# Optimization experiments

Hardware: AMD Instinct MI355X
Metric: run time of the kernel (lower is better)

## Reference

```python
import jax, jax.numpy as jnp
import numpy as np

N_NODES = 100000


def sage_conv(x, src, dst, W_l, b_l, W_r):
    # PyG SAGEConv (aggr='mean'): out = lin_l(mean_j x_j) + lin_r(x_i)
    msg = x[src]  # [E, d] gather of source-node features
    agg = jax.ops.segment_sum(msg, dst, num_segments=N_NODES)  # [N, d]
    deg = jax.ops.segment_sum(jnp.ones((src.shape[0],), x.dtype), dst,
                              num_segments=N_NODES)
    mean = agg / jnp.clip(deg, 1.0, None)[:, None]
    return mean @ W_l.T + b_l + x @ W_r.T


def setup_inputs() -> dict:
    key = jax.random.key(0)
    ks = jax.random.split(key, 12)
    d_in, d_h, d_out, n_edges = 64, 64, 2, 1200000
    s = 1.0 / np.sqrt(d_h)
    inp = {
        "x": jax.random.normal(ks[0], (N_NODES, d_in), dtype=jnp.float32),
        "edge_index": jax.random.randint(ks[1], (2, n_edges), 0, N_NODES,
                                         dtype=jnp.int64),
        "W_l1": jax.random.uniform(ks[2], (d_h, d_in), jnp.float32, -s, s),
        "b_l1": jax.random.uniform(ks[3], (d_h,), jnp.float32, -s, s),
        "W_r1": jax.random.uniform(ks[4], (d_h, d_in), jnp.float32, -s, s),
        "W_l2": jax.random.uniform(ks[5], (d_h, d_h), jnp.float32, -s, s),
        "b_l2": jax.random.uniform(ks[6], (d_h,), jnp.float32, -s, s),
        "W_r2": jax.random.uniform(ks[7], (d_h, d_h), jnp.float32, -s, s),
        "W_c": jax.random.uniform(ks[8], (d_out, d_h), jnp.float32, -s, s),
        "b_c": jax.random.uniform(ks[9], (d_out,), jnp.float32, -s, s),
    }
    return inp


def reference(x, edge_index, W_l1, b_l1, W_r1, W_l2, b_l2, W_r2, W_c, b_c):
    src, dst = edge_index[0], edge_index[1]
    # layer 1 + relu (dropout is identity in eval mode)
    h = jax.nn.relu(sage_conv(x, src, dst, W_l1, b_l1, W_r1))
    # layer 2 (no relu per forward())
    h = sage_conv(h, src, dst, W_l2, b_l2, W_r2)
    # classifier
    return h @ W_c.T + b_c
```

## Files before the change

kernel.cpp:

```cpp
#include <hip/hip_runtime.h>

#define N_NODES 100000
#define D 64
#define NTILES 3125
#define NBUCK 391
#define NBLK_A 256
#define GCNT_N (NBUCK * NBLK_A)
#define NCHUNK ((GCNT_N + 255) / 256)
#define NTILE_T (N_NODES / 32)
#define TROW 72
#define TBLK 512

typedef __attribute__((ext_vector_type(8))) short short8;
typedef __attribute__((ext_vector_type(16))) float f32x16;
union Pack8 { uint4 u; short8 s; };

__device__ __forceinline__ unsigned f2bf(float f) {
  unsigned u = __float_as_uint(f);
  return (u + 0x7fffu + ((u >> 16) & 1u)) >> 16;
}
#define BF_LO(u) __uint_as_float(((unsigned)(u)) << 16)
#define BF_HI(u) __uint_as_float(((unsigned)(u)) & 0xffff0000u)



__global__ __launch_bounds__(256) void passA_count(const int* __restrict__ dst,
                                                   int* __restrict__ gcnt,
                                                   int nE, int ec) {
  __shared__ int cnt[NBUCK];
  int t = threadIdx.x, blk = blockIdx.x;
  for (int i = t; i < NBUCK; i += 256) cnt[i] = 0;
  __syncthreads();
  int e0 = blk * ec, e1 = min(e0 + ec, nE);
  for (int e = e0 + t; e < e1; e += 256) atomicAdd(&cnt[dst[e] >> 8], 1);
  __syncthreads();
  for (int b = t; b < NBUCK; b += 256) gcnt[b * NBLK_A + blk] = cnt[b];
}

__global__ void gscan_p1(const int* __restrict__ g, int* __restrict__ csum) {
  int t = threadIdx.x, b = blockIdx.x;
  int i = b * 256 + t;
  int v = (i < GCNT_N) ? g[i] : 0;
  for (int off = 32; off; off >>= 1) v += __shfl_down(v, off);
  __shared__ int ws4[4];
  if ((t & 63) == 0) ws4[t >> 6] = v;
  __syncthreads();
  if (t == 0) csum[b] = ws4[0] + ws4[1] + ws4[2] + ws4[3];
}

__global__ void gscan_p2(int* __restrict__ csum, int nB) {
  __shared__ int s[1024];
  int t = threadIdx.x;
  int orig = (t < nB) ? csum[t] : 0;
  s[t] = orig;
  __syncthreads();
  for (int off = 1; off < 1024; off <<= 1) {
    int v = (t >= off) ? s[t - off] : 0;
    __syncthreads();
    s[t] += v;
    __syncthreads();
  }
  if (t < nB) csum[t] = s[t] - orig;
}

__global__ void gscan_p3(int* __restrict__ g, const int* __restrict__ csum) {
  __shared__ int s[256];
  int t = threadIdx.x, b = blockIdx.x;
  int i = b * 256 + t;
  int d = (i < GCNT_N) ? g[i] : 0;
  s[t] = d;
  __syncthreads();
  for (int off = 1; off < 256; off <<= 1) {
    int v = (t >= off) ? s[t - off] : 0;
    __syncthreads();
    s[t] += v;
    __syncthreads();
  }
  if (i < GCNT_N) g[i] = s[t] - d + csum[b];
}

__global__ __launch_bounds__(256) void passC_prep(
    const int* __restrict__ src, const int* __restrict__ dst,
    const int* __restrict__ S, unsigned* __restrict__ pairs4, int nE, int ec,
    const float* __restrict__ Wc, const float* __restrict__ Wl2,
    const float* __restrict__ Wr2, const float* __restrict__ bl2,
    const float* __restrict__ bc, const float* __restrict__ Wl1,
    const float* __restrict__ Wr1, float* __restrict__ A2,
    float* __restrict__ B2, float* __restrict__ bfv,
    unsigned short* __restrict__ wcat) {
  __shared__ int cur[NBUCK];
  int t = threadIdx.x, blk = blockIdx.x;
  if (blk < NBLK_A) {
    for (int b = t; b < NBUCK; b += 256) cur[b] = S[b * NBLK_A + blk];
    __syncthreads();
    int e0 = blk * ec, e1 = min(e0 + ec, nE);
    for (int e = e0 + t; e < e1; e += 256) {
      int d = dst[e];
      int p = atomicAdd(&cur[d >> 8], 1);
      pairs4[p] = ((unsigned)(d & 255) << 24) | (unsigned)src[e];
    }
  } else {
    for (int i = t; i < 8192; i += 256)
      wcat[i] = (unsigned short)f2bf((i < 4096) ? Wl1[i] : Wr1[i - 4096]);
    if (t < 128) {
      int c = t >> 6, k = t & 63;
      float sa = 0.f, sb = 0.f;
      for (int j = 0; j < 64; ++j) {
        float w = Wc[c * 64 + j];
        sa = fmaf(w, Wl2[j * 64 + k], sa);
        sb = fmaf(w, Wr2[j * 64 + k], sb);
      }
      A2[c * 64 + k] = sa;
      B2[c * 64 + k] = sb;
    }
    if (t < 2) {
      float s = bc[t];
      for (int j = 0; j < 64; ++j) s = fmaf(Wc[t * 64 + j], bl2[j], s);
      bfv[t] = s;
    }
  }
}

__global__ __launch_bounds__(256) void passD_transform(
    const unsigned* __restrict__ pairs4, const int* __restrict__ S,
    int* __restrict__ tstart, unsigned* __restrict__ srt4, int nE,
    const float* __restrict__ x, const unsigned short* __restrict__ wcat,
    const float* __restrict__ bl, unsigned short* __restrict__ t1,
    unsigned short* __restrict__ r1b) {
  __shared__ int h8[8 * 16];
  __shared__ int ex8[9];
  __shared__ int cur8[8];
  int t = threadIdx.x;
  if (blockIdx.x < NBUCK) {
    int b = blockIdx.x;
    int base = S[b * NBLK_A];
    int end = (b == NBUCK - 1) ? nE : S[(b + 1) * NBLK_A];
    if (t < 128) h8[t] = 0;
    __syncthreads();
    for (int p = base + t; p < end; p += 256)
      atomicAdd(&h8[((pairs4[p] >> 29) & 7) * 16 + (t & 15)], 1);
    __syncthreads();
    if (t == 0) {
      int run = base;
      for (int bin = 0; bin < 8; ++bin) {
        ex8[bin] = run;
        int s = 0;
        for (int i = 0; i < 16; ++i) s += h8[bin * 16 + i];
        run += s;
      }
      ex8[8] = run;
    }
    __syncthreads();
    if (t < 8) {
      cur8[t] = ex8[t];
      tstart[b * 8 + t] = ex8[t];
    }
    if (b == NBUCK - 1 && t == 0) tstart[NBUCK * 8] = nE;
    __syncthreads();
    for (int p = base + t; p < end; p += 256) {
      unsigned pk = pairs4[p];
      int slot = atomicAdd(&cur8[(pk >> 29) & 7], 1);
      srt4[slot] = pk;
    }
  } else {
    int lane = t & 63;
    int l31 = lane & 31, hi = lane >> 5;

    short8 af[4][4];
#pragma unroll
    for (int jt = 0; jt < 4; ++jt)
#pragma unroll
      for (int kk = 0; kk < 4; ++kk)
        af[jt][kk] =
            *(const short8*)(wcat + (jt * 32 + l31) * 64 + kk * 16 + 8 * hi);

    const f32x16 Z = {0.f, 0.f, 0.f, 0.f, 0.f, 0.f, 0.f, 0.f,
                      0.f, 0.f, 0.f, 0.f, 0.f, 0.f, 0.f, 0.f};
    const float4* x4 = (const float4*)x;

    int gw = ((blockIdx.x - NBUCK) * 256 + t) >> 6;
    int nW = (TBLK * 256) >> 6;

    for (int tile = gw; tile < NTILE_T; tile += nW) {
      int node = tile * 32 + l31;
      f32x16 acc[4] = {Z, Z, Z, Z};
#pragma unroll
      for (int kk = 0; kk < 4; ++kk) {
        float4 fa = x4[(size_t)node * 16 + kk * 4 + 2 * hi];
        float4 fb = x4[(size_t)node * 16 + kk * 4 + 2 * hi + 1];
        Pack8 pk;
        pk.u.x = f2bf(fa.x) | (f2bf(fa.y) << 16);
        pk.u.y = f2bf(fa.z) | (f2bf(fa.w) << 16);
        pk.u.z = f2bf(fb.x) | (f2bf(fb.y) << 16);
        pk.u.w = f2bf(fb.z) | (f2bf(fb.w) << 16);
        acc[0] = __builtin_amdgcn_mfma_f32_32x32x16_bf16(af[0][kk], pk.s, acc[0], 0, 0, 0);
        acc[1] = __builtin_amdgcn_mfma_f32_32x32x16_bf16(af[1][kk], pk.s, acc[1], 0, 0, 0);
        acc[2] = __builtin_amdgcn_mfma_f32_32x32x16_bf16(af[2][kk], pk.s, acc[2], 0, 0, 0);
        acc[3] = __builtin_amdgcn_mfma_f32_32x32x16_bf16(af[3][kk], pk.s, acc[3], 0, 0, 0);
      }
#pragma unroll
      for (int jt = 0; jt < 2; ++jt)
#pragma unroll
        for (int rg = 0; rg < 4; ++rg) {
          int j0 = jt * 32 + 8 * rg + 4 * hi;
          uint2 p;
          p.x = f2bf(acc[jt][4 * rg + 0]) | (f2bf(acc[jt][4 * rg + 1]) << 16);
          p.y = f2bf(acc[jt][4 * rg + 2]) | (f2bf(acc[jt][4 * rg + 3]) << 16);
          *(uint2*)(t1 + (size_t)node * 64 + j0) = p;
        }
#pragma unroll
      for (int jt = 2; jt < 4; ++jt)
#pragma unroll
        for (int rg = 0; rg < 4; ++rg) {
          int j0 = (jt - 2) * 32 + 8 * rg + 4 * hi;
          float4 bv = ((const float4*)bl)[j0 >> 2];
          uint2 p;
          p.x = f2bf(acc[jt][4 * rg + 0] + bv.x) |
                (f2bf(acc[jt][4 * rg + 1] + bv.y) << 16);
          p.y = f2bf(acc[jt][4 * rg + 2] + bv.z) |
                (f2bf(acc[jt][4 * rg + 3] + bv.w) << 16);
          *(uint2*)(r1b + (size_t)node * 64 + j0) = p;
        }
    }
  }
}

__global__ __launch_bounds__(256) void tile_g1(
    const unsigned* __restrict__ srt4, const int* __restrict__ tstart,
    const unsigned short* __restrict__ t1,
    const unsigned short* __restrict__ r1b, const float* __restrict__ A2,
    const float* __restrict__ B2, float2* __restrict__ g2,
    float2* __restrict__ s2, int nE) {
  __shared__ float pAB[4][64];
  __shared__ unsigned short stg[4][2][16 * TROW];
  __shared__ int ideg[4][64];
  int t = threadIdx.x, lane = t & 63, w = t >> 6;
  pAB[t >> 6][t & 63] = (t < 128) ? A2[t] : B2[t - 128];
  __syncthreads();

  int tile = blockIdx.x;
  int base = tstart[tile];
  int end = tstart[tile + 1];
  int l31 = lane & 31, hi = lane >> 5;
  int o = lane >> 3, j8 = lane & 7;
  unsigned short* stA = &stg[w][0][0];
  unsigned short* stB = &stg[w][1][0];

  int ngAll = (end > base) ? ((end - base + 15) >> 4) : 0;
  int gper = (ngAll + 3) >> 2;
  int wbase = base + min(w * gper, ngAll) * 16;
  int wend = min(base + min((w + 1) * gper, ngAll) * 16, end);

  const f32x16 Z = {0.f, 0.f, 0.f, 0.f, 0.f, 0.f, 0.f, 0.f,
                    0.f, 0.f, 0.f, 0.f, 0.f, 0.f, 0.f, 0.f};
  f32x16 acc0 = Z, acc1 = Z;
  int degc = 0;
  int ng = (wend > wbase) ? ((wend - wbase + 15) >> 4) : 0;

  unsigned pkA = 0u, pkB = 0u;
  int cntA = 0, cntB = 0;
  uint4 vA0 = make_uint4(0, 0, 0, 0), vA1 = vA0, vB0 = vA0, vB1 = vA0;
  if (ng > 0) {
    pkA = srt4[min(wbase + (lane & 15), nE - 1)];
    cntA = min(wend - wbase, 16);
    int s0 = __shfl((int)pkA, o) & 0xFFFFFF;
    int s1 = __shfl((int)pkA, 8 + o) & 0xFFFFFF;
    vA0 = *(const uint4*)(t1 + (size_t)((o < cntA) ? s0 : 0) * 64 + j8 * 8);
    vA1 = *(const uint4*)(t1 + (size_t)((8 + o < cntA) ? s1 : 0) * 64 + j8 * 8);
  }
  if (ng > 1) {
    int nb = wbase + 16;
    pkB = srt4[min(nb + (lane & 15), nE - 1)];
    cntB = min(wend - nb, 16);
    int s0 = __shfl((int)pkB, o) & 0xFFFFFF;
    int s1 = __shfl((int)pkB, 8 + o) & 0xFFFFFF;
    vB0 = *(const uint4*)(t1 + (size_t)((o < cntB) ? s0 : 0) * 64 + j8 * 8);
    vB1 = *(const uint4*)(t1 + (size_t)((8 + o < cntB) ? s1 : 0) * 64 + j8 * 8);
  }

  for (int gg = 0; gg < ng; gg += 2) {
    bool hasB = (gg + 1 < ng);
    *(uint4*)(stA + o * TROW + j8 * 8) = vA0;
    *(uint4*)(stA + (8 + o) * TROW + j8 * 8) = vA1;
    if (hasB) {
      *(uint4*)(stB + o * TROW + j8 * 8) = vB0;
      *(uint4*)(stB + (8 + o) * TROW + j8 * 8) = vB1;
    }
    unsigned amA[8], amB[8];
#pragma unroll
    for (int m = 0; m < 8; ++m) {
      int e = 8 * hi + m;
      int pv = __shfl((int)pkA, e);
      bool ok = (e < cntA) && (((pv >> 24) & 31) == l31);
      amA[m] = ok ? 0x3F80u : 0u;
      degc += (amA[m] >> 7) & 1;
    }
    if (hasB) {
#pragma unroll
      for (int m = 0; m < 8; ++m) {
        int e = 8 * hi + m;
        int pv = __shfl((int)pkB, e);
        bool ok = (e < cntB) && (((pv >> 24) & 31) == l31);
        amB[m] = ok ? 0x3F80u : 0u;
        degc += (amB[m] >> 7) & 1;
      }
    }
    if (gg + 2 < ng) {
      int nb = wbase + (gg + 2) * 16;
      pkA = srt4[min(nb + (lane & 15), nE - 1)];
      cntA = min(wend - nb, 16);
      int s0 = __shfl((int)pkA, o) & 0xFFFFFF;
      int s1 = __shfl((int)pkA, 8 + o) & 0xFFFFFF;
      vA0 = *(const uint4*)(t1 + (size_t)((o < cntA) ? s0 : 0) * 64 + j8 * 8);
      vA1 = *(const uint4*)(t1 + (size_t)((8 + o < cntA) ? s1 : 0) * 64 + j8 * 8);
    }
    if (gg + 3 < ng) {
      int nb = wbase + (gg + 3) * 16;
      pkB = srt4[min(nb + (lane & 15), nE - 1)];
      cntB = min(wend - nb, 16);
      int s0 = __shfl((int)pkB, o) & 0xFFFFFF;
      int s1 = __shfl((int)pkB, 8 + o) & 0xFFFFFF;
      vB0 = *(const uint4*)(t1 + (size_t)((o < cntB) ? s0 : 0) * 64 + j8 * 8);
      vB1 = *(const uint4*)(t1 + (size_t)((8 + o < cntB) ? s1 : 0) * 64 + j8 * 8);
    }
    {
      Pack8 I;
      I.u.x = amA[0] | (amA[1] << 16);
      I.u.y = amA[2] | (amA[3] << 16);
      I.u.z = amA[4] | (amA[5] << 16);
      I.u.w = amA[6] | (amA[7] << 16);
      unsigned short b0[8], b1[8];
#pragma unroll
      for (int m = 0; m < 8; ++m) {
        b0[m] = stA[(8 * hi + m) * TROW + l31];
        b1[m] = stA[(8 * hi + m) * TROW + 32 + l31];
      }
      Pack8 F0, F1;
      F0.u.x = b0[0] | ((unsigned)b0[1] << 16);
      F0.u.y = b0[2] | ((unsigned)b0[3] << 16);
      F0.u.z = b0[4] | ((unsigned)b0[5] << 16);
      F0.u.w = b0[6] | ((unsigned)b0[7] << 16);
      F1.u.x = b1[0] | ((unsigned)b1[1] << 16);
      F1.u.y = b1[2] | ((unsigned)b1[3] << 16);
      F1.u.z = b1[4] | ((unsigned)b1[5] << 16);
      F1.u.w = b1[6] | ((unsigned)b1[7] << 16);
      acc0 = __builtin_amdgcn_mfma_f32_32x32x16_bf16(F0.s, I.s, acc0, 0, 0, 0);
      acc1 = __builtin_amdgcn_mfma_f32_32x32x16_bf16(F1.s, I.s, acc1, 0, 0, 0);
    }
    if (hasB) {
      Pack8 I;
      I.u.x = amB[0] | (amB[1] << 16);
      I.u.y = amB[2] | (amB[3] << 16);
      I.u.z = amB[4] | (amB[5] << 16);
      I.u.w = amB[6] | (amB[7] << 16);
      unsigned short b0[8], b1[8];
#pragma unroll
      for (int m = 0; m < 8; ++m) {
        b0[m] = stB[(8 * hi + m) * TROW + l31];
        b1[m] = stB[(8 * hi + m) * TROW + 32 + l31];
      }
      Pack8 F0, F1;
      F0.u.x = b0[0] | ((unsigned)b0[1] << 16);
      F0.u.y = b0[2] | ((unsigned)b0[3] << 16);
      F0.u.z = b0[4] | ((unsigned)b0[5] << 16);
      F0.u.w = b0[6] | ((unsigned)b0[7] << 16);
      F1.u.x = b1[0] | ((unsigned)b1[1] << 16);
      F1.u.y = b1[2] | ((unsigned)b1[3] << 16);
      F1.u.z = b1[4] | ((unsigned)b1[5] << 16);
      F1.u.w = b1[6] | ((unsigned)b1[7] << 16);
      acc0 = __builtin_amdgcn_mfma_f32_32x32x16_bf16(F0.s, I.s, acc0, 0, 0, 0);
      acc1 = __builtin_amdgcn_mfma_f32_32x32x16_bf16(F1.s, I.s, acc1, 0, 0, 0);
    }
  }

  ideg[w][lane] = degc;
  __syncthreads();
  float* red = (float*)&stg[0][0][0];
  for (int r = 1; r < 4; ++r) {
    if (w == r) {
#pragma unroll
      for (int i = 0; i < 16; ++i) {
        red[i * 64 + lane] = acc0[i];
        red[(16 + i) * 64 + lane] = acc1[i];
      }
    }
    __syncthreads();
    if (w == 0) {
#pragma unroll
      for (int i = 0; i < 16; ++i) {
        acc0[i] += red[i * 64 + lane];
        acc1[i] += red[(16 + i) * 64 + lane];
      }
    }
    __syncthreads();
  }

  if (w == 0) {
    int dtot = ideg[0][lane] + ideg[1][lane] + ideg[2][lane] + ideg[3][lane];
    float degf = (float)(dtot + __shfl_xor(dtot, 32));
    float inv = 1.f / fmaxf(degf, 1.f);
    int node = tile * 32 + l31;
    float d0 = 0.f, d1 = 0.f, d2 = 0.f, d3 = 0.f;
#pragma unroll
    for (int fb = 0; fb < 2; ++fb) {
#pragma unroll
      for (int q4 = 0; q4 < 4; ++q4) {
        int f0 = fb * 32 + q4 * 8 + 4 * hi;
        uint2 rv = *(const uint2*)(r1b + (size_t)node * 64 + f0);
        float bias[4] = {BF_LO(rv.x), BF_HI(rv.x), BF_LO(rv.y), BF_HI(rv.y)};
#pragma unroll
        for (int j = 0; j < 4; ++j) {
          float a = fb ? acc1[q4 * 4 + j] : acc0[q4 * 4 + j];
          float hv = fmaxf(fmaf(a, inv, bias[j]), 0.f);
          int f = f0 + j;
          d0 = fmaf(hv, pAB[0][f], d0);
          d1 = fmaf(hv, pAB[1][f], d1);
          d2 = fmaf(hv, pAB[2][f], d2);
          d3 = fmaf(hv, pAB[3][f], d3);
        }
      }
    }
    d0 += __shfl_xor(d0, 32);
    d1 += __shfl_xor(d1, 32);
    d2 += __shfl_xor(d2, 32);
    d3 += __shfl_xor(d3, 32);
    if (hi == 0) {
      g2[node] = make_float2(d0, d1);
      s2[node] = make_float2(d2, d3);
    }
  }
}

__global__ __launch_bounds__(256) void bucket_g2(
    const unsigned* __restrict__ pairs4, const int* __restrict__ S,
    const float2* __restrict__ g2, const float2* __restrict__ s2,
    const float* __restrict__ bfv, float* __restrict__ out, int nE) {
  __shared__ float o0[256], o1[256];
  __shared__ int cnt[256];
  int t = threadIdx.x, b = blockIdx.x;
  o0[t] = 0.f;
  o1[t] = 0.f;
  cnt[t] = 0;
  __syncthreads();
  int base = S[b * NBLK_A];
  int end = (b == NBUCK - 1) ? nE : S[(b + 1) * NBLK_A];
  for (int p = base + t; p < end; p += 256) {
    unsigned pk = pairs4[p];
    float2 v = g2[pk & 0xFFFFFFu];
    int dl = pk >> 24;
    atomicAdd(&o0[dl], v.x);
    atomicAdd(&o1[dl], v.y);
    atomicAdd(&cnt[dl], 1);
  }
  __syncthreads();
  int node = b * 256 + t;
  if (node < N_NODES) {
    float inv = 1.f / (float)max(cnt[t], 1);
    float2 sv = s2[node];
    out[(size_t)node * 2 + 0] = fmaf(o0[t], inv, sv.x) + bfv[0];
    out[(size_t)node * 2 + 1] = fmaf(o1[t], inv, sv.y) + bfv[1];
  }
}

extern "C" void kernel_launch(void* const* d_in, const int* in_sizes, int n_in,
                              void* d_out, int out_size, void* d_ws,
                              size_t ws_size, hipStream_t stream) {
  const float* x   = (const float*)d_in[0];
  const int*   ei  = (const int*)d_in[1];
  const float* Wl1 = (const float*)d_in[2];
  const float* bl1 = (const float*)d_in[3];
  const float* Wr1 = (const float*)d_in[4];
  const float* Wl2 = (const float*)d_in[5];
  const float* bl2 = (const float*)d_in[6];
  const float* Wr2 = (const float*)d_in[7];
  const float* Wc  = (const float*)d_in[8];
  const float* bc  = (const float*)d_in[9];
  float* out = (float*)d_out;

  int nE = in_sizes[1] / 2;
  const int* src = ei;
  const int* dst = ei + nE;

  unsigned* pairs4 = (unsigned*)d_ws;
  unsigned* srt4 = pairs4 + nE;
  unsigned short* t1 = (unsigned short*)(srt4 + nE);
  unsigned short* r1b = t1 + (size_t)N_NODES * D;
  float2* g2 = (float2*)(r1b + (size_t)N_NODES * D);
  float2* s2 = g2 + N_NODES;
  float* A2 = (float*)(s2 + N_NODES);
  float* B2 = A2 + 128;
  float* bfv = B2 + 128;
  unsigned short* wcat = (unsigned short*)(bfv + 4);
  int* tstart = (int*)(wcat + 8192);
  int* gcnt = tstart + (NBUCK * 8 + 2);
  int* csum = gcnt + GCNT_N;

  int ec = (nE + NBLK_A - 1) / NBLK_A;

  passA_count<<<NBLK_A, 256, 0, stream>>>(dst, gcnt, nE, ec);
  gscan_p1<<<NCHUNK, 256, 0, stream>>>(gcnt, csum);
  gscan_p2<<<1, 1024, 0, stream>>>(csum, NCHUNK);
  gscan_p3<<<NCHUNK, 256, 0, stream>>>(gcnt, csum);
  passC_prep<<<NBLK_A + 1, 256, 0, stream>>>(src, dst, gcnt, pairs4, nE, ec,
                                             Wc, Wl2, Wr2, bl2, bc, Wl1, Wr1,
                                             A2, B2, bfv, wcat);
  passD_transform<<<NBUCK + TBLK, 256, 0, stream>>>(pairs4, gcnt, tstart,
                                                    srt4, nE, x, wcat, bl1,
                                                    t1, r1b);
  tile_g1<<<NTILES, 256, 0, stream>>>(srt4, tstart, t1, r1b, A2, B2, g2, s2,
                                      nE);
  bucket_g2<<<NBUCK, 256, 0, stream>>>(pairs4, gcnt, g2, s2, bfv, out, nE);
}
```

Baseline: 124.5 us.

## Replace three-kernel global scan with atomic bucket offsets and in-block scan

Each counting block now reserves its slot within each bucket by atomically adding its count to a per-bucket total, which yields a per-block offset directly. The three separate scan kernels are removed, and the scatter kernel instead does a small 391-entry prefix scan in shared memory in every block to get bucket base addresses. This cuts two kernel launches and the global scan traffic, at the cost of a memset, global atomics, and a redundant per-block scan. Edge order within a bucket now depends on atomic arrival order, so results may differ slightly between runs through float summation order.

```diff
diff --git a/kernel.cpp b/kernel.cpp
--- a/kernel.cpp
+++ b/kernel.cpp
@@ -6,7 +6,6 @@
 #define NBUCK 391
 #define NBLK_A 256
 #define GCNT_N (NBUCK * NBLK_A)
-#define NCHUNK ((GCNT_N + 255) / 256)
 #define NTILE_T (N_NODES / 32)
 #define TROW 72
 #define TBLK 512
@@ -23,9 +22,9 @@
 #define BF_HI(u) __uint_as_float(((unsigned)(u)) & 0xffff0000u)
 
 
-
 __global__ __launch_bounds__(256) void passA_count(const int* __restrict__ dst,
-                                                   int* __restrict__ gcnt,
+                                                   int* __restrict__ goff,
+                                                   int* __restrict__ btot,
                                                    int nE, int ec) {
   __shared__ int cnt[NBUCK];
   int t = threadIdx.x, blk = blockIdx.x;
@@ -34,54 +33,14 @@
   int e0 = blk * ec, e1 = min(e0 + ec, nE);
   for (int e = e0 + t; e < e1; e += 256) atomicAdd(&cnt[dst[e] >> 8], 1);
   __syncthreads();
-  for (int b = t; b < NBUCK; b += 256) gcnt[b * NBLK_A + blk] = cnt[b];
-}
-
-__global__ void gscan_p1(const int* __restrict__ g, int* __restrict__ csum) {
-  int t = threadIdx.x, b = blockIdx.x;
-  int i = b * 256 + t;
-  int v = (i < GCNT_N) ? g[i] : 0;
-  for (int off = 32; off; off >>= 1) v += __shfl_down(v, off);
-  __shared__ int ws4[4];
-  if ((t & 63) == 0) ws4[t >> 6] = v;
-  __syncthreads();
-  if (t == 0) csum[b] = ws4[0] + ws4[1] + ws4[2] + ws4[3];
-}
-
-__global__ void gscan_p2(int* __restrict__ csum, int nB) {
-  __shared__ int s[1024];
-  int t = threadIdx.x;
-  int orig = (t < nB) ? csum[t] : 0;
-  s[t] = orig;
-  __syncthreads();
-  for (int off = 1; off < 1024; off <<= 1) {
-    int v = (t >= off) ? s[t - off] : 0;
-    __syncthreads();
-    s[t] += v;
-    __syncthreads();
-  }
-  if (t < nB) csum[t] = s[t] - orig;
-}
-
-__global__ void gscan_p3(int* __restrict__ g, const int* __restrict__ csum) {
-  __shared__ int s[256];
-  int t = threadIdx.x, b = blockIdx.x;
-  int i = b * 256 + t;
-  int d = (i < GCNT_N) ? g[i] : 0;
-  s[t] = d;
-  __syncthreads();
-  for (int off = 1; off < 256; off <<= 1) {
-    int v = (t >= off) ? s[t - off] : 0;
-    __syncthreads();
-    s[t] += v;
-    __syncthreads();
-  }
-  if (i < GCNT_N) g[i] = s[t] - d + csum[b];
+  for (int b = t; b < NBUCK; b += 256)
+    goff[b * NBLK_A + blk] = atomicAdd(&btot[b], cnt[b]);
 }
 
 __global__ __launch_bounds__(256) void passC_prep(
     const int* __restrict__ src, const int* __restrict__ dst,
-    const int* __restrict__ S, unsigned* __restrict__ pairs4, int nE, int ec,
+    const int* __restrict__ goff, const int* __restrict__ btot,
+    int* __restrict__ bstart, unsigned* __restrict__ pairs4, int nE, int ec,
     const float* __restrict__ Wc, const float* __restrict__ Wl2,
     const float* __restrict__ Wr2, const float* __restrict__ bl2,
     const float* __restrict__ bc, const float* __restrict__ Wl1,
@@ -89,9 +48,25 @@
     float* __restrict__ B2, float* __restrict__ bfv,
     unsigned short* __restrict__ wcat) {
   __shared__ int cur[NBUCK];
+  __shared__ int sa[512], sb[512];
   int t = threadIdx.x, blk = blockIdx.x;
   if (blk < NBLK_A) {
-    for (int b = t; b < NBUCK; b += 256) cur[b] = S[b * NBLK_A + blk];
+    for (int i = t; i < 512; i += 256) sa[i] = (i < NBUCK) ? btot[i] : 0;
+    __syncthreads();
+    int* A = sa;
+    int* B = sb;
+    for (int off = 1; off < 512; off <<= 1) {
+      for (int i = t; i < 512; i += 256)
+        B[i] = A[i] + ((i >= off) ? A[i - off] : 0);
+      __syncthreads();
+      int* tmp = A; A = B; B = tmp;
+    }
+    for (int b = t; b < NBUCK; b += 256) {
+      int base = (b == 0) ? 0 : A[b - 1];
+      cur[b] = base + goff[b * NBLK_A + blk];
+      if (blk == 0) bstart[b] = base;
+    }
+    if (blk == 0 && t == 0) bstart[NBUCK] = A[NBUCK - 1];
     __syncthreads();
     int e0 = blk * ec, e1 = min(e0 + ec, nE);
     for (int e = e0 + t; e < e1; e += 256) {
@@ -104,14 +79,14 @@
       wcat[i] = (unsigned short)f2bf((i < 4096) ? Wl1[i] : Wr1[i - 4096]);
     if (t < 128) {
       int c = t >> 6, k = t & 63;
-      float sa = 0.f, sb = 0.f;
+      float sa2 = 0.f, sb2 = 0.f;
       for (int j = 0; j < 64; ++j) {
         float w = Wc[c * 64 + j];
-        sa = fmaf(w, Wl2[j * 64 + k], sa);
-        sb = fmaf(w, Wr2[j * 64 + k], sb);
-      }
-      A2[c * 64 + k] = sa;
-      B2[c * 64 + k] = sb;
+        sa2 = fmaf(w, Wl2[j * 64 + k], sa2);
+        sb2 = fmaf(w, Wr2[j * 64 + k], sb2);
+      }
+      A2[c * 64 + k] = sa2;
+      B2[c * 64 + k] = sb2;
     }
     if (t < 2) {
       float s = bc[t];
@@ -122,7 +97,7 @@
 }
 
 __global__ __launch_bounds__(256) void passD_transform(
-    const unsigned* __restrict__ pairs4, const int* __restrict__ S,
+    const unsigned* __restrict__ pairs4, const int* __restrict__ bstart,
     int* __restrict__ tstart, unsigned* __restrict__ srt4, int nE,
     const float* __restrict__ x, const unsigned short* __restrict__ wcat,
     const float* __restrict__ bl, unsigned short* __restrict__ t1,
@@ -133,8 +108,8 @@
   int t = threadIdx.x;
   if (blockIdx.x < NBUCK) {
     int b = blockIdx.x;
-    int base = S[b * NBLK_A];
-    int end = (b == NBUCK - 1) ? nE : S[(b + 1) * NBLK_A];
+    int base = bstart[b];
+    int end = bstart[b + 1];
     if (t < 128) h8[t] = 0;
     __syncthreads();
     for (int p = base + t; p < end; p += 256)
@@ -432,7 +407,7 @@
 }
 
 __global__ __launch_bounds__(256) void bucket_g2(
-    const unsigned* __restrict__ pairs4, const int* __restrict__ S,
+    const unsigned* __restrict__ pairs4, const int* __restrict__ bstart,
     const float2* __restrict__ g2, const float2* __restrict__ s2,
     const float* __restrict__ bfv, float* __restrict__ out, int nE) {
   __shared__ float o0[256], o1[256];
@@ -442,8 +417,8 @@
   o1[t] = 0.f;
   cnt[t] = 0;
   __syncthreads();
-  int base = S[b * NBLK_A];
-  int end = (b == NBUCK - 1) ? nE : S[(b + 1) * NBLK_A];
+  int base = bstart[b];
+  int end = bstart[b + 1];
   for (int p = base + t; p < end; p += 256) {
     unsigned pk = pairs4[p];
     float2 v = g2[pk & 0xFFFFFFu];
@@ -492,22 +467,22 @@
   float* bfv = B2 + 128;
   unsigned short* wcat = (unsigned short*)(bfv + 4);
   int* tstart = (int*)(wcat + 8192);
-  int* gcnt = tstart + (NBUCK * 8 + 2);
-  int* csum = gcnt + GCNT_N;
+  int* goff = tstart + (NBUCK * 8 + 2);
+  int* btot = goff + GCNT_N;
+  int* bstart = btot + (NBUCK + 1);
 
   int ec = (nE + NBLK_A - 1) / NBLK_A;
 
-  passA_count<<<NBLK_A, 256, 0, stream>>>(dst, gcnt, nE, ec);
-  gscan_p1<<<NCHUNK, 256, 0, stream>>>(gcnt, csum);
-  gscan_p2<<<1, 1024, 0, stream>>>(csum, NCHUNK);
-  gscan_p3<<<NCHUNK, 256, 0, stream>>>(gcnt, csum);
-  passC_prep<<<NBLK_A + 1, 256, 0, stream>>>(src, dst, gcnt, pairs4, nE, ec,
-                                             Wc, Wl2, Wr2, bl2, bc, Wl1, Wr1,
-                                             A2, B2, bfv, wcat);
-  passD_transform<<<NBUCK + TBLK, 256, 0, stream>>>(pairs4, gcnt, tstart,
+  hipMemsetAsync(btot, 0, (NBUCK + 1) * sizeof(int), stream);
+  passA_count<<<NBLK_A, 256, 0, stream>>>(dst, goff, btot, nE, ec);
+  passC_prep<<<NBLK_A + 1, 256, 0, stream>>>(src, dst, goff, btot, bstart,
+                                             pairs4, nE, ec, Wc, Wl2, Wr2,
+                                             bl2, bc, Wl1, Wr1, A2, B2, bfv,
+                                             wcat);
+  passD_transform<<<NBUCK + TBLK, 256, 0, stream>>>(pairs4, bstart, tstart,
                                                     srt4, nE, x, wcat, bl1,
                                                     t1, r1b);
   tile_g1<<<NTILES, 256, 0, stream>>>(srt4, tstart, t1, r1b, A2, B2, g2, s2,
                                       nE);
-  bucket_g2<<<NBUCK, 256, 0, stream>>>(pairs4, gcnt, g2, s2, bfv, out, nE);
-}
+  bucket_g2<<<NBUCK, 256, 0, stream>>>(pairs4, bstart, g2, s2, bfv, out, nE);
+}
```

Measured after the change: 137.5 us. 10.4% more time.
